# Performance work log

Hardware: AMD Instinct MI355X
Metric: run time of the kernel (lower is better)

## Reference

```python
import jax, jax.numpy as jnp
import numpy as np

VOCAB = 100000
D = 128
B = 256
L = 2048  # leaves per tree (power of two -> complete binary tree)


def setup_inputs() -> dict:
    key = jax.random.key(0)
    k1, k2, k3, k4 = jax.random.split(key, 4)
    word_ids = jax.random.randint(k1, (B, L), 0, VOCAB)
    embedding = jax.random.normal(k2, (VOCAB, D), dtype=jnp.float32) * 0.1
    # torch nn.Linear(2*D, D): weight [D, 2*D], bias [D]
    W = jax.random.normal(k3, (D, 2 * D), dtype=jnp.float32) * (1.0 / np.sqrt(2 * D))
    b = jax.random.normal(k4, (D,), dtype=jnp.float32) * 0.01
    return {"word_ids": word_ids, "embedding": embedding, "W": W, "b": b}


def reference(word_ids, embedding, W, b):
    # Leaves: embedding lookup for every leaf of every tree. [B, L, D]
    x = embedding[word_ids]
    # Internal nodes, batched by depth: each level combines adjacent pairs
    # via linear(concat(left, right)). log2(L) levels (static unroll).
    while x.shape[1] > 1:
        left = x[:, 0::2, :]   # [B, n/2, D]
        right = x[:, 1::2, :]  # [B, n/2, D]
        pair = jnp.concatenate([left, right], axis=-1)  # [B, n/2, 2D]
        x = jnp.einsum('bnd,od->bno', pair, W) + b      # [B, n/2, D]
    return x[:, 0, :]  # root result per tree, [B, D]
```

## Files before the change

### kernel.cpp

```cpp
#include <hip/hip_runtime.h>


typedef __bf16 bf16x8 __attribute__((ext_vector_type(8)));
typedef __bf16 bf16x4 __attribute__((ext_vector_type(4)));
typedef float f32x4 __attribute__((ext_vector_type(4)));

#define STRIDE 136

__global__ void pack_w_kernel(const float* __restrict__ W,
                              __bf16* __restrict__ wpack) {
    const int f = blockIdx.x;
    const int tid = threadIdx.x;
    const int wv = tid >> 6, l = tid & 63;
    const int nl = f >> 3, kk = f & 7;
    const int o = ((wv << 1) + nl) * 16 + (l & 15);
    const int d = kk * 32 + ((l >> 4) << 3);
    const float* src = W + o * 256 + d;
    bf16x8 h;
#pragma unroll
    for (int j = 0; j < 8; ++j) h[j] = (__bf16)src[j];
    *(bf16x8*)(wpack + (size_t)(f * 256 + tid) * 8) = h;
}

template <int NOUT>
__device__ __forceinline__ void level_step(
    const __bf16* src0, const __bf16* src1, __bf16* dst,
    const bf16x8* wf, const float* bval, int wv, int q, int lm)
{
    const int ntm = (NOUT + 15) >> 4;
#pragma unroll
    for (int mt = 0; mt < ntm; ++mt) {
        const __bf16* src = mt ? src1 : src0;
        const int me = (NOUT >= 16) ? lm : (lm < NOUT ? lm : 0);
        bf16x8 af[8];
#pragma unroll
        for (int kk = 0; kk < 8; ++kk) {
            const int hi = kk >> 2;
            const int col = (kk & 3) * 32 + q * 8;
            const int row = 2 * me + hi;
            af[kk] = *(const bf16x8*)&src[row * STRIDE + col];
        }
#pragma unroll
        for (int nl = 0; nl < 2; ++nl) {
            f32x4 acc = { bval[nl], bval[nl], bval[nl], bval[nl] };
#pragma unroll
            for (int kk = 0; kk < 8; ++kk)
                acc = __builtin_amdgcn_mfma_f32_16x16x32_bf16(
                    af[kk], wf[nl * 8 + kk], acc, 0, 0, 0);
            const int col = (2 * wv + nl) * 16 + lm;
            const bf16x4 hv = __builtin_convertvector(acc, bf16x4);
#pragma unroll
            for (int r = 0; r < 4; ++r) {
                const int row = mt * 16 + q * 4 + r;
                if (row < NOUT)
                    dst[row * STRIDE + col] = hv[r];
            }
        }
    }
    __syncthreads();
}

__device__ __forceinline__ void level_final(
    const __bf16* src, __bf16* yrow,
    const bf16x8* wf, const float* bval, int wv, int q, int lm)
{
    const int me = (lm < 2) ? lm : 0;
    bf16x8 af[8];
#pragma unroll
    for (int kk = 0; kk < 8; ++kk) {
        const int hi = kk >> 2;
        const int col = (kk & 3) * 32 + q * 8;
        af[kk] = *(const bf16x8*)&src[(2 * me + hi) * STRIDE + col];
    }
#pragma unroll
    for (int nl = 0; nl < 2; ++nl) {
        f32x4 acc = { bval[nl], bval[nl], bval[nl], bval[nl] };
#pragma unroll
        for (int kk = 0; kk < 8; ++kk)
            acc = __builtin_amdgcn_mfma_f32_16x16x32_bf16(
                af[kk], wf[nl * 8 + kk], acc, 0, 0, 0);
        const int col = (2 * wv + nl) * 16 + lm;
        if (q == 0) {
            yrow[0 * 128 + col] = (__bf16)acc[0];
            yrow[1 * 128 + col] = (__bf16)acc[1];
        }
    }
}

__global__ __launch_bounds__(256, 3) void tree128_kernel(
    const int* __restrict__ wid, const float* __restrict__ emb,
    const __bf16* __restrict__ wpack, const float* __restrict__ bias,
    __bf16* __restrict__ yout)
{
    __shared__ __align__(16) __bf16 bufA[128 * STRIDE];
    __shared__ __align__(16) __bf16 bufB[32 * STRIDE];
    const int tid = threadIdx.x;
    const int batch = blockIdx.x >> 4;
    const int grp = blockIdx.x & 15;
    const int wv = tid >> 6, ln = tid & 63, q = ln >> 4, lm = ln & 15;

    bf16x8 wf[16];
    const bf16x8* wp = (const bf16x8*)wpack;
#pragma unroll
    for (int f = 0; f < 16; ++f) wf[f] = wp[f * 256 + tid];
    float bval[2];
    bval[0] = bias[(2 * wv + 0) * 16 + lm];
    bval[1] = bias[(2 * wv + 1) * 16 + lm];

    const int* wb = wid + batch * 2048 + grp * 128;
    int idreg[16];
#pragma unroll
    for (int i = 0; i < 16; ++i) idreg[i] = wb[(tid >> 5) + 8 * i];

#pragma unroll
    for (int i = 0; i < 16; ++i) {
        const int row = (tid >> 5) + 8 * i;
        const int c4 = tid & 31;
        const f32x4 v = *(const f32x4*)(emb + (size_t)idreg[i] * 128 + c4 * 4);
        *(bf16x4*)&bufA[row * STRIDE + c4 * 4] =
            __builtin_convertvector(v, bf16x4);
    }
    __syncthreads();

    __bf16* A = bufA;
    __bf16* B = bufB;
    level_step<32>(A,               A + 32 * STRIDE, B,              wf, bval, wv, q, lm);
    level_step<32>(A + 64 * STRIDE, A + 96 * STRIDE, A,              wf, bval, wv, q, lm);
    level_step<32>(B,               A,               A + 32 * STRIDE,wf, bval, wv, q, lm);
    level_step<16>(A + 32 * STRIDE, nullptr,         B,              wf, bval, wv, q, lm);
    level_step<8> (B,               nullptr,         A,              wf, bval, wv, q, lm);
    level_step<4> (A,               nullptr,         B,              wf, bval, wv, q, lm);
    level_final(B, yout + (size_t)(batch * 32 + grp * 2) * 128,
                wf, bval, wv, q, lm);
}

__global__ __launch_bounds__(256) void tree32_kernel(
    const __bf16* __restrict__ yin, const __bf16* __restrict__ wpack,
    const float* __restrict__ bias, float* __restrict__ out)
{
    __shared__ __align__(16) __bf16 buf[2][32 * STRIDE];
    const int tid = threadIdx.x;
    const int batch = blockIdx.x;
    const int wv = tid >> 6, ln = tid & 63, q = ln >> 4, lm = ln & 15;

    bf16x8 wf[16];
    const bf16x8* wp = (const bf16x8*)wpack;
#pragma unroll
    for (int f = 0; f < 16; ++f) wf[f] = wp[f * 256 + tid];
    float bval[2];
    bval[0] = bias[(2 * wv + 0) * 16 + lm];
    bval[1] = bias[(2 * wv + 1) * 16 + lm];

#pragma unroll
    for (int i = 0; i < 2; ++i) {
        const int flat = tid + 256 * i;
        const int row = flat >> 4;
        const int c8 = flat & 15;
        const bf16x8 v =
            *(const bf16x8*)(yin + (size_t)(batch * 32 + row) * 128 + c8 * 8);
        *(bf16x8*)&buf[0][row * STRIDE + c8 * 8] = v;
    }
    __syncthreads();

    int nin = 32, rb = 0;
    while (nin > 1) {
        const int nout = nin >> 1;
        const int me = (lm < nout) ? lm : 0;
        bf16x8 af[8];
#pragma unroll
        for (int kk = 0; kk < 8; ++kk) {
            const int hi = kk >> 2;
            const int col = (kk & 3) * 32 + q * 8;
            af[kk] = *(const bf16x8*)&buf[rb][(2 * me + hi) * STRIDE + col];
        }
#pragma unroll
        for (int nl = 0; nl < 2; ++nl) {
            f32x4 acc = { bval[nl], bval[nl], bval[nl], bval[nl] };
#pragma unroll
            for (int kk = 0; kk < 8; ++kk)
                acc = __builtin_amdgcn_mfma_f32_16x16x32_bf16(
                    af[kk], wf[nl * 8 + kk], acc, 0, 0, 0);
            const int col = (2 * wv + nl) * 16 + lm;
            if (nout == 1) {
                if (q == 0) out[(size_t)batch * 128 + col] = acc[0];
            } else {
                const bf16x4 hv = __builtin_convertvector(acc, bf16x4);
#pragma unroll
                for (int r = 0; r < 4; ++r) {
                    const int row = q * 4 + r;
                    if (row < nout)
                        buf[rb ^ 1][row * STRIDE + col] = hv[r];
                }
            }
        }
        __syncthreads();
        rb ^= 1;
        nin = nout;
    }
}

extern "C" void kernel_launch(void* const* d_in, const int* in_sizes, int n_in,
                              void* d_out, int out_size, void* d_ws, size_t ws_size,
                              hipStream_t stream) {
    const int*   wid = (const int*)d_in[0];
    const float* emb = (const float*)d_in[1];
    const float* W   = (const float*)d_in[2];
    const float* b   = (const float*)d_in[3];
    float* out = (float*)d_out;

    __bf16* wpack = (__bf16*)d_ws;
    __bf16* y     = wpack + 32768;

    pack_w_kernel<<<16, 256, 0, stream>>>(W, wpack);
    tree128_kernel<<<4096, 256, 0, stream>>>(wid, emb, wpack, b, y);
    tree32_kernel<<<256, 256, 0, stream>>>(y, wpack, b, out);
}
```

Measured before the change: 130.9 us.

## Repartition tree MFMA tiles across waves and swizzle shared-memory layout

```diff
diff --git a/kernel.cpp b/kernel.cpp
--- a/kernel.cpp
+++ b/kernel.cpp
@@ -5,84 +5,82 @@
 typedef __bf16 bf16x4 __attribute__((ext_vector_type(4)));
 typedef float f32x4 __attribute__((ext_vector_type(4)));
 
-#define STRIDE 136
+__device__ __forceinline__ int sw_off(int row, int col) {
+    return row * 128 + ((((col >> 3) ^ (row & 15)) << 3) | (col & 7));
+}
 
 __global__ void pack_w_kernel(const float* __restrict__ W,
                               __bf16* __restrict__ wpack) {
-    const int f = blockIdx.x;
-    const int tid = threadIdx.x;
-    const int wv = tid >> 6, l = tid & 63;
-    const int nl = f >> 3, kk = f & 7;
-    const int o = ((wv << 1) + nl) * 16 + (l & 15);
+    const int gf = blockIdx.x;
+    const int l = threadIdx.x;
+    const int nt = gf >> 3, kk = gf & 7;
+    const int o = nt * 16 + (l & 15);
     const int d = kk * 32 + ((l >> 4) << 3);
     const float* src = W + o * 256 + d;
     bf16x8 h;
 #pragma unroll
     for (int j = 0; j < 8; ++j) h[j] = (__bf16)src[j];
-    *(bf16x8*)(wpack + (size_t)(f * 256 + tid) * 8) = h;
+    *(bf16x8*)(wpack + (size_t)(gf * 64 + l) * 8) = h;
 }
 
 template <int NOUT>
-__device__ __forceinline__ void level_step(
-    const __bf16* src0, const __bf16* src1, __bf16* dst,
-    const bf16x8* wf, const float* bval, int wv, int q, int lm)
-{
-    const int ntm = (NOUT + 15) >> 4;
-#pragma unroll
-    for (int mt = 0; mt < ntm; ++mt) {
-        const __bf16* src = mt ? src1 : src0;
-        const int me = (NOUT >= 16) ? lm : (lm < NOUT ? lm : 0);
-        bf16x8 af[8];
-#pragma unroll
-        for (int kk = 0; kk < 8; ++kk) {
-            const int hi = kk >> 2;
-            const int col = (kk & 3) * 32 + q * 8;
-            const int row = 2 * me + hi;
-            af[kk] = *(const bf16x8*)&src[row * STRIDE + col];
-        }
-#pragma unroll
-        for (int nl = 0; nl < 2; ++nl) {
-            f32x4 acc = { bval[nl], bval[nl], bval[nl], bval[nl] };
-#pragma unroll
-            for (int kk = 0; kk < 8; ++kk)
-                acc = __builtin_amdgcn_mfma_f32_16x16x32_bf16(
-                    af[kk], wf[nl * 8 + kk], acc, 0, 0, 0);
-            const int col = (2 * wv + nl) * 16 + lm;
-            const bf16x4 hv = __builtin_convertvector(acc, bf16x4);
-#pragma unroll
-            for (int r = 0; r < 4; ++r) {
-                const int row = mt * 16 + q * 4 + r;
-                if (row < NOUT)
-                    dst[row * STRIDE + col] = hv[r];
-            }
-        }
-    }
-    __syncthreads();
-}
-
-__device__ __forceinline__ void level_final(
-    const __bf16* src, __bf16* yrow,
-    const bf16x8* wf, const float* bval, int wv, int q, int lm)
+__device__ __forceinline__ void step_tile(
+    const __bf16* __restrict__ src, __bf16* __restrict__ dst,
+    const bf16x8* wf, const float* bval, int nw, int q, int lm)
+{
+    const int me = (NOUT >= 16) ? lm : (lm < NOUT ? lm : 0);
+    f32x4 acc[4];
+#pragma unroll
+    for (int nl = 0; nl < 4; ++nl)
+        acc[nl] = (f32x4){ bval[nl], bval[nl], bval[nl], bval[nl] };
+#pragma unroll
+    for (int kk = 0; kk < 8; ++kk) {
+        const int row = 2 * me + (kk >> 2);
+        const int col = (kk & 3) * 32 + q * 8;
+        const bf16x8 af = *(const bf16x8*)&src[sw_off(row, col)];
+#pragma unroll
+        for (int nl = 0; nl < 4; ++nl)
+            acc[nl] = __builtin_amdgcn_mfma_f32_16x16x32_bf16(
+                af, wf[nl * 8 + kk], acc[nl], 0, 0, 0);
+    }
+#pragma unroll
+    for (int nl = 0; nl < 4; ++nl) {
+        const int col = (nw * 4 + nl) * 16 + lm;
+        const bf16x4 hv = __builtin_convertvector(acc[nl], bf16x4);
+#pragma unroll
+        for (int r = 0; r < 4; ++r) {
+            const int row = q * 4 + r;
+            if (NOUT >= 16 || row < NOUT)
+                dst[sw_off(row, col)] = hv[r];
+        }
+    }
+}
+
+__device__ __forceinline__ void final_tile(
+    const __bf16* __restrict__ src, __bf16* __restrict__ yrow,
+    const bf16x8* wf, const float* bval, int nw, int q, int lm)
 {
     const int me = (lm < 2) ? lm : 0;
-    bf16x8 af[8];
+    f32x4 acc[4];
+#pragma unroll
+    for (int nl = 0; nl < 4; ++nl)
+        acc[nl] = (f32x4){ bval[nl], bval[nl], bval[nl], bval[nl] };
 #pragma unroll
     for (int kk = 0; kk < 8; ++kk) {
-        const int hi = kk >> 2;
+        const int row = 2 * me + (kk >> 2);
         const int col = (kk & 3) * 32 + q * 8;
-        af[kk] = *(const bf16x8*)&src[(2 * me + hi) * STRIDE + col];
-    }
-#pragma unroll
-    for (int nl = 0; nl < 2; ++nl) {
-        f32x4 acc = { bval[nl], bval[nl], bval[nl], bval[nl] };
-#pragma unroll
-        for (int kk = 0; kk < 8; ++kk)
-            acc = __builtin_amdgcn_mfma_f32_16x16x32_bf16(
-                af[kk], wf[nl * 8 + kk], acc, 0, 0, 0);
-        const int col = (2 * wv + nl) * 16 + lm;
+        const bf16x8 af = *(const bf16x8*)&src[sw_off(row, col)];
+#pragma unroll
+        for (int nl = 0; nl < 4; ++nl)
+            acc[nl] = __builtin_amdgcn_mfma_f32_16x16x32_bf16(
+                af, wf[nl * 8 + kk], acc[nl], 0, 0, 0);
+    }
+#pragma unroll
+    for (int nl = 0; nl < 4; ++nl) {
+        const int col = (nw * 4 + nl) * 16 + lm;
         if (q == 0) {
-            yrow[0 * 128 + col] = (__bf16)acc[0];
-            yrow[1 * 128 + col] = (__bf16)acc[1];
+            yrow[0 * 128 + col] = (__bf16)acc[nl][0];
+            yrow[1 * 128 + col] = (__bf16)acc[nl][1];
         }
     }
 }
@@ -92,48 +90,61 @@
     const __bf16* __restrict__ wpack, const float* __restrict__ bias,
     __bf16* __restrict__ yout)
 {
-    __shared__ __align__(16) __bf16 bufA[128 * STRIDE];
-    __shared__ __align__(16) __bf16 bufB[32 * STRIDE];
+    __shared__ __align__(16) __bf16 A[128 * 128];
+    __shared__ __align__(16) __bf16 S[32 * 128];
     const int tid = threadIdx.x;
     const int batch = blockIdx.x >> 4;
     const int grp = blockIdx.x & 15;
-    const int wv = tid >> 6, ln = tid & 63, q = ln >> 4, lm = ln & 15;
-
-    bf16x8 wf[16];
+    const int wv = tid >> 6, nw = wv & 1, mw = wv >> 1;
+    const int ln = tid & 63, q = ln >> 4, lm = ln & 15;
+
+    {
+        const int* wb = wid + batch * 2048 + grp * 128;
+        int idreg[16];
+#pragma unroll
+        for (int i = 0; i < 16; ++i) idreg[i] = wb[(tid >> 5) + 8 * i];
+#pragma unroll
+        for (int i = 0; i < 16; ++i) {
+            const int row = (tid >> 5) + 8 * i;
+            const int c4 = tid & 31;
+            const f32x4 v =
+                *(const f32x4*)(emb + (size_t)idreg[i] * 128 + c4 * 4);
+            *(bf16x4*)&A[sw_off(row, c4 * 4)] =
+                __builtin_convertvector(v, bf16x4);
+        }
+    }
+
+    bf16x8 wf[32];
     const bf16x8* wp = (const bf16x8*)wpack;
 #pragma unroll
-    for (int f = 0; f < 16; ++f) wf[f] = wp[f * 256 + tid];
-    float bval[2];
-    bval[0] = bias[(2 * wv + 0) * 16 + lm];
-    bval[1] = bias[(2 * wv + 1) * 16 + lm];
-
-    const int* wb = wid + batch * 2048 + grp * 128;
-    int idreg[16];
-#pragma unroll
-    for (int i = 0; i < 16; ++i) idreg[i] = wb[(tid >> 5) + 8 * i];
-
-#pragma unroll
-    for (int i = 0; i < 16; ++i) {
-        const int row = (tid >> 5) + 8 * i;
-        const int c4 = tid & 31;
-        const f32x4 v = *(const f32x4*)(emb + (size_t)idreg[i] * 128 + c4 * 4);
-        *(bf16x4*)&bufA[row * STRIDE + c4 * 4] =
-            __builtin_convertvector(v, bf16x4);
-    }
-    __syncthreads();
-
-    __bf16* A = bufA;
-    __bf16* B = bufB;
-    level_step<32>(A,               A + 32 * STRIDE, B,              wf, bval, wv, q, lm);
-    level_step<32>(A + 64 * STRIDE, A + 96 * STRIDE, A,              wf, bval, wv, q, lm);
-    level_step<32>(B,               A,               A + 32 * STRIDE,wf, bval, wv, q, lm);
-    level_step<16>(A + 32 * STRIDE, nullptr,         B,              wf, bval, wv, q, lm);
-    level_step<8> (B,               nullptr,         A,              wf, bval, wv, q, lm);
-    level_step<4> (A,               nullptr,         B,              wf, bval, wv, q, lm);
-    level_final(B, yout + (size_t)(batch * 32 + grp * 2) * 128,
-                wf, bval, wv, q, lm);
-}
-
+    for (int f = 0; f < 32; ++f) wf[f] = wp[(nw * 32 + f) * 64 + ln];
+    float bval[4];
+#pragma unroll
+    for (int nl = 0; nl < 4; ++nl) bval[nl] = bias[(nw * 4 + nl) * 16 + lm];
+
+    __syncthreads();
+
+    step_tile<16>(A + (mw ? 32 * 128 : 0), S + (mw ? 16 * 128 : 0),
+                  wf, bval, nw, q, lm);
+    __syncthreads();
+    step_tile<16>(A + (mw ? 96 * 128 : 64 * 128), A + (mw ? 16 * 128 : 0),
+                  wf, bval, nw, q, lm);
+    __syncthreads();
+    step_tile<16>(mw ? A : S, A + (mw ? 48 * 128 : 32 * 128),
+                  wf, bval, nw, q, lm);
+    __syncthreads();
+    if (mw == 0) step_tile<16>(A + 32 * 128, S, wf, bval, nw, q, lm);
+    __syncthreads();
+    if (mw == 0) step_tile<8>(S, A, wf, bval, nw, q, lm);
+    __syncthreads();
+    if (mw == 0) step_tile<4>(A, S, wf, bval, nw, q, lm);
+    __syncthreads();
+    if (mw == 0)
+        final_tile(S, yout + (size_t)(batch * 32 + grp * 2) * 128,
+                   wf, bval, nw, q, lm);
+}
+
+#define STRIDE 136
 __global__ __launch_bounds__(256) void tree32_kernel(
     const __bf16* __restrict__ yin, const __bf16* __restrict__ wpack,
     const float* __restrict__ bias, float* __restrict__ out)
@@ -146,7 +157,7 @@
     bf16x8 wf[16];
     const bf16x8* wp = (const bf16x8*)wpack;
 #pragma unroll
-    for (int f = 0; f < 16; ++f) wf[f] = wp[f * 256 + tid];
+    for (int f = 0; f < 16; ++f) wf[f] = wp[(16 * wv + f) * 64 + ln];
     float bval[2];
     bval[0] = bias[(2 * wv + 0) * 16 + lm];
     bval[1] = bias[(2 * wv + 1) * 16 + lm];
@@ -211,7 +222,7 @@
     __bf16* wpack = (__bf16*)d_ws;
     __bf16* y     = wpack + 32768;
 
-    pack_w_kernel<<<16, 256, 0, stream>>>(W, wpack);
+    pack_w_kernel<<<64, 64, 0, stream>>>(W, wpack);
     tree128_kernel<<<4096, 256, 0, stream>>>(wid, emb, wpack, b, y);
     tree32_kernel<<<256, 256, 0, stream>>>(y, wpack, b, out);
 }
```

After: 386.3 us. 195% more time.
